# Performance work log

Hardware: AMD Instinct MI355X
Metric: run time of the kernel (lower is better)

Reference implementation:

```python
import jax, jax.numpy as jnp
import numpy as np
import math

N = 50000       # nodes
E = 800000      # edges
C_IN = 64
C_OUT = 32
N_SH = 9        # (l_max+1)^2 with l_max=2
H = 32          # radial_hidden_dim


def spherical_harmonics(vectors):
    # vectors: [..., 3] -> [..., 9]; faithful to source incl. (x+iy).real == x
    norm = jnp.clip(jnp.linalg.norm(vectors, axis=-1, keepdims=True), 1e-8)
    d = vectors / norm
    x, y, z = d[..., 0], d[..., 1], d[..., 2]
    c00 = 0.5 / math.sqrt(math.pi)
    c1 = 0.5 * math.sqrt(3.0 / (2.0 * math.pi))
    c1z = 0.5 * math.sqrt(3.0 / math.pi)
    c2 = 0.25 * math.sqrt(15.0 / (2.0 * math.pi))
    c2z = 0.5 * math.sqrt(15.0 / (2.0 * math.pi))
    c20 = 0.25 * math.sqrt(5.0 / math.pi)
    feats = [
        c00 * jnp.ones_like(x),
        -c1 * x,                      # -0.5*sqrt(3/2pi)*(x+iy).real
        c1z * z,
        c1 * x,                       # 0.5*sqrt(3/2pi)*(x-iy).real
        c2 * (x * x - y * y),         # 0.25*sqrt(15/2pi)*((x+iy)^2).real
        -c2z * z * x,
        c20 * (2.0 * z * z - x * x - y * y),
        c2z * z * x,
        c2 * (x * x - y * y),
    ]
    return jnp.stack(feats, axis=-1)


def setup_inputs() -> dict:
    key = jax.random.key(0)
    ks = jax.random.split(key, 9)
    features = jax.random.normal(ks[0], (N, C_IN), dtype=jnp.float32)
    positions = jax.random.normal(ks[1], (N, 3), dtype=jnp.float32)
    edge_index = jax.random.randint(ks[2], (2, E), 0, N, dtype=jnp.int64)
    fan1 = N_SH + C_IN  # 73 (intended fan-in of first radial layer)
    W1 = jax.random.normal(ks[3], (fan1, H), dtype=jnp.float32) / math.sqrt(fan1)
    b1 = jnp.zeros((H,), dtype=jnp.float32)
    W2 = jax.random.normal(ks[4], (H, H), dtype=jnp.float32) / math.sqrt(H)
    b2 = jnp.zeros((H,), dtype=jnp.float32)
    W3 = jax.random.normal(ks[5], (H, N_SH * C_OUT), dtype=jnp.float32) / math.sqrt(H)
    b3 = jnp.zeros((N_SH * C_OUT,), dtype=jnp.float32)
    return {"features": features, "positions": positions, "W1": W1, "b1": b1,
            "W2": W2, "b2": b2, "W3": W3, "b3": b3, "edge_index": edge_index}


def reference(features, positions, W1, b1, W2, b2, W3, b3, edge_index):
    row, col = edge_index[0], edge_index[1]
    rel_pos = positions[row] - positions[col]                 # [E,3]
    dist = jnp.clip(jnp.linalg.norm(rel_pos, axis=-1, keepdims=True), 1e-8)
    directions = rel_pos / dist
    y_ij = spherical_harmonics(directions)                    # [E,9]
    combined = jnp.concatenate([y_ij, features[col]], axis=-1)  # [E,9+C_IN]
    h = jax.nn.silu(combined @ W1 + b1)
    h = jax.nn.silu(h @ W2 + b2)
    messages = h @ W3 + b3                                    # [E,9*C_OUT]
    msg = messages.reshape(-1, N_SH, C_OUT).sum(axis=1)       # [E,C_OUT]
    out = jax.ops.segment_sum(msg, row, num_segments=features.shape[0])
    return out
```

## Files before the change

kernel.cpp:

```cpp
#include <hip/hip_runtime.h>
#include <hip/hip_fp16.h>

#define NNODES 50000
#define NEDGES 800000
#define CIN 64
#define COUT 32
#define NSH 9
#define HDIM 32

#define NT_BLOCKS 6250
#define HIST_BLOCKS 782
#define SCAN_BLOCKS 125
#define SCAN_CHUNK 400

__device__ __forceinline__ void prep_body(
    int t, const float* __restrict__ W3, const float* __restrict__ b3,
    const float* __restrict__ W1, const float* __restrict__ b1,
    float* __restrict__ W3s, float* __restrict__ b3s, float* __restrict__ prm)
{
    if (t < HDIM * COUT) {
        int k = t >> 5, c = t & 31;
        float s = 0.f;
        #pragma unroll
        for (int q = 0; q < NSH; ++q) s += W3[k * (NSH * COUT) + q * COUT + c];
        W3s[t] = s;
    }
    if (t < COUT) {
        float s = 0.f;
        #pragma unroll
        for (int q = 0; q < NSH; ++q) s += b3[q * COUT + t];
        b3s[t] = s;
    }
    if (t < HDIM) {
        const float c00 = 0.28209479177387814f;
        const float c1  = 0.3454941494713355f;
        const float c1z = 0.4886025119029199f;
        const float c2  = 0.38627420202318958f;
        const float c2z = 0.7725484040463791f;
        const float c20 = 0.31539156525252005f;
        prm[t]       = b1[t] + c00 * W1[0 * HDIM + t];
        prm[32 + t]  = c1  * (W1[3 * HDIM + t] - W1[1 * HDIM + t]);
        prm[64 + t]  = c1z *  W1[2 * HDIM + t];
        prm[96 + t]  = c2z * (W1[7 * HDIM + t] - W1[5 * HDIM + t]);
        prm[128 + t] = c2  * (W1[4 * HDIM + t] + W1[8 * HDIM + t]);
        prm[160 + t] = c20 *  W1[6 * HDIM + t];
    }
}

__global__ void prep_w3(const float* __restrict__ W3, const float* __restrict__ b3,
                        const float* __restrict__ W1, const float* __restrict__ b1,
                        float* __restrict__ W3s, float* __restrict__ b3s,
                        float* __restrict__ prm) {
    prep_body(threadIdx.x, W3, b3, W1, b1, W3s, b3s, prm);
}

__global__ __launch_bounds__(256) void nt_hist(
    const float* __restrict__ feat, const float* __restrict__ W1,
    const int* __restrict__ ei, float* __restrict__ g1,
    int* __restrict__ cnt, int do_nt)
{
    int b = blockIdx.x;
    if (do_nt && b < NT_BLOCKS) {
        int tid = b * 256 + threadIdx.x;
        int n = tid >> 5, c = tid & 31;
        if (n < NNODES) {
            float acc = 0.f;
            const float* fr = feat + (size_t)n * CIN;
            const float* wp = W1 + NSH * HDIM + c;
            #pragma unroll 8
            for (int k = 0; k < CIN; ++k)
                acc = fmaf(fr[k], wp[k * HDIM], acc);
            g1[(size_t)n * HDIM + c] = acc;
        }
    } else {
        int hb = do_nt ? (b - NT_BLOCKS) : b;
        int e4 = (hb * 256 + threadIdx.x) * 4;
        if (e4 < NEDGES) {
            int4 r = *reinterpret_cast<const int4*>(ei + e4);
            atomicAdd(&cnt[r.x], 1);
            atomicAdd(&cnt[r.y], 1);
            atomicAdd(&cnt[r.z], 1);
            atomicAdd(&cnt[r.w], 1);
        }
    }
}

__global__ __launch_bounds__(256) void scan_bsum(const int* __restrict__ cnt,
                                                 int* __restrict__ bsum) {
    int b = blockIdx.x, t = threadIdx.x;
    int base = b * SCAN_CHUNK;
    int s = 0;
    for (int i = t; i < SCAN_CHUNK; i += 256) s += cnt[base + i];
    #pragma unroll
    for (int d = 32; d > 0; d >>= 1) s += __shfl_down(s, d);
    __shared__ int l4[4];
    if ((t & 63) == 0) l4[t >> 6] = s;
    __syncthreads();
    if (t == 0) bsum[b] = l4[0] + l4[1] + l4[2] + l4[3];
}

__global__ __launch_bounds__(1024) void scan_top_prep(
    const int* __restrict__ bsum, int* __restrict__ ebsum, int* __restrict__ off,
    const float* __restrict__ W3, const float* __restrict__ b3,
    const float* __restrict__ W1, const float* __restrict__ b1,
    float* __restrict__ W3s, float* __restrict__ b3s, float* __restrict__ prm)
{
    if (blockIdx.x == 1) {
        prep_body(threadIdx.x, W3, b3, W1, b1, W3s, b3s, prm);
        return;
    }
    __shared__ int lds[128];
    int t = threadIdx.x;
    if (t < 128) lds[t] = (t < SCAN_BLOCKS) ? bsum[t] : 0;
    __syncthreads();
    for (int d = 1; d < 128; d <<= 1) {
        int u = (t >= d && t < 128) ? lds[t - d] : 0;
        __syncthreads();
        if (t < 128) lds[t] += u;
        __syncthreads();
    }
    if (t < SCAN_BLOCKS) ebsum[t] = (t == 0) ? 0 : lds[t - 1];
    if (t == 0) off[NNODES] = NEDGES;
}

__global__ __launch_bounds__(256) void scan_offsets(const int* __restrict__ cnt,
                                                    const int* __restrict__ ebsum,
                                                    int* __restrict__ off,
                                                    int* __restrict__ cursor) {
    int b = blockIdx.x, t = threadIdx.x;
    int base = b * SCAN_CHUNK;
    __shared__ int lds[256];
    int2 c2 = make_int2(0, 0);
    if (t < SCAN_CHUNK / 2) c2 = reinterpret_cast<const int2*>(cnt + base)[t];
    int ps = c2.x + c2.y;
    lds[t] = ps;
    __syncthreads();
    for (int d = 1; d < 256; d <<= 1) {
        int u = (t >= d) ? lds[t - d] : 0;
        __syncthreads();
        lds[t] += u;
        __syncthreads();
    }
    int excl = lds[t] - ps;
    if (t < SCAN_CHUNK / 2) {
        int o = ebsum[b] + excl;
        int2 w = make_int2(o, o + c2.x);
        reinterpret_cast<int2*>(off + base)[t] = w;
        reinterpret_cast<int2*>(cursor + base)[t] = w;
    }
}

__global__ __launch_bounds__(256) void edge_compute_g1(
    const float* __restrict__ g1, const float* __restrict__ pos,
    const float* __restrict__ prm,
    const float* __restrict__ W2, const float* __restrict__ b2,
    const float* __restrict__ W3s, const float* __restrict__ b3s,
    const int* __restrict__ ei, int* __restrict__ cursor,
    unsigned int* __restrict__ msg)
{
    int e = blockIdx.x * blockDim.x + threadIdx.x;
    if (e >= NEDGES) return;
    int row = ei[e];
    int col = ei[NEDGES + e];

    int slot = atomicAdd(&cursor[row], 1);
    unsigned int* mp = msg + (size_t)slot * 16;

    float px = pos[3 * row + 0] - pos[3 * col + 0];
    float py = pos[3 * row + 1] - pos[3 * col + 1];
    float pz = pos[3 * row + 2] - pos[3 * col + 2];
    float dist = fmaxf(sqrtf(px * px + py * py + pz * pz), 1e-8f);
    float inv = 1.0f / dist;
    float dx = px * inv, dy = py * inv, dz = pz * inv;
    float n2 = fmaxf(sqrtf(dx * dx + dy * dy + dz * dz), 1e-8f);
    float i2 = 1.0f / n2;
    float x = dx * i2, y = dy * i2, z = dz * i2;

    float zx = z * x;
    float xxyy = x * x - y * y;
    float w6 = 2.f * z * z - x * x - y * y;

    const float* b1e = prm;
    const float* A = prm + 32;
    const float* B = prm + 64;
    const float* C = prm + 96;
    const float* D = prm + 128;
    const float* E = prm + 160;

    float h1[HDIM];
    const float4* g4 = reinterpret_cast<const float4*>(g1 + (size_t)col * HDIM);
    #pragma unroll
    for (int q = 0; q < 8; ++q) {
        float4 g = g4[q];
        h1[4 * q + 0] = g.x; h1[4 * q + 1] = g.y;
        h1[4 * q + 2] = g.z; h1[4 * q + 3] = g.w;
    }
    #pragma unroll
    for (int c = 0; c < HDIM; ++c) {
        float v = h1[c] + b1e[c];
        v = fmaf(x, A[c], v);
        v = fmaf(z, B[c], v);
        v = fmaf(zx, C[c], v);
        v = fmaf(xxyy, D[c], v);
        v = fmaf(w6, E[c], v);
        h1[c] = v / (1.f + __expf(-v));
    }

    float h2[HDIM];
    #pragma unroll
    for (int c = 0; c < HDIM; ++c) h2[c] = b2[c];
    for (int k = 0; k < HDIM; ++k) {
        float v = h1[k];
        #pragma unroll
        for (int c = 0; c < HDIM; ++c) h2[c] = fmaf(v, W2[k * HDIM + c], h2[c]);
    }
    #pragma unroll
    for (int c = 0; c < HDIM; ++c) {
        float v = h2[c];
        h2[c] = v / (1.f + __expf(-v));
    }

    float m[COUT];
    #pragma unroll
    for (int c = 0; c < COUT; ++c) m[c] = b3s[c];
    for (int k = 0; k < HDIM; ++k) {
        float v = h2[k];
        #pragma unroll
        for (int c = 0; c < COUT; ++c) m[c] = fmaf(v, W3s[k * COUT + c], m[c]);
    }

    uint4 pk[4];
    unsigned int* pu = reinterpret_cast<unsigned int*>(pk);
    #pragma unroll
    for (int q = 0; q < 16; ++q) {
        __half2 hh = __floats2half2_rn(m[2 * q], m[2 * q + 1]);
        pu[q] = *reinterpret_cast<unsigned int*>(&hh);
    }
    uint4* mp4 = reinterpret_cast<uint4*>(mp);
    #pragma unroll
    for (int q = 0; q < 4; ++q) mp4[q] = pk[q];
}

__global__ __launch_bounds__(256) void gather_kernel(
    const unsigned int* __restrict__ msg, const int* __restrict__ off,
    float* __restrict__ out)
{
    int node = blockIdx.x * 4 + (threadIdx.x >> 6);
    if (node >= NNODES) return;
    int lane = threadIdx.x & 63;
    int g = lane >> 4, p = lane & 15;
    int s0 = off[node], s1 = off[node + 1];
    float ax = 0.f, ay = 0.f;
    for (int s = s0 + g; s < s1; s += 4) {
        unsigned int u = msg[(size_t)s * 16 + p];
        __half2 h = *reinterpret_cast<__half2*>(&u);
        ax += __low2float(h);
        ay += __high2float(h);
    }
    ax += __shfl_xor(ax, 16); ay += __shfl_xor(ay, 16);
    ax += __shfl_xor(ax, 32); ay += __shfl_xor(ay, 32);
    if (lane < 16)
        reinterpret_cast<float2*>(out + (size_t)node * COUT)[p] = make_float2(ax, ay);
}

__global__ __launch_bounds__(256) void edge_atomic_kernel(
    const float* __restrict__ feat, const float* __restrict__ pos,
    const float* __restrict__ W1, const float* __restrict__ b1,
    const float* __restrict__ W2, const float* __restrict__ b2,
    const float* __restrict__ W3s, const float* __restrict__ b3s,
    const int* __restrict__ ei, float* __restrict__ out)
{
    int e = blockIdx.x * blockDim.x + threadIdx.x;
    if (e >= NEDGES) return;
    int row = ei[e];
    int col = ei[NEDGES + e];

    float px = pos[3 * row + 0] - pos[3 * col + 0];
    float py = pos[3 * row + 1] - pos[3 * col + 1];
    float pz = pos[3 * row + 2] - pos[3 * col + 2];
    float dist = fmaxf(sqrtf(px * px + py * py + pz * pz), 1e-8f);
    float inv = 1.0f / dist;
    float dx = px * inv, dy = py * inv, dz = pz * inv;
    float n2 = fmaxf(sqrtf(dx * dx + dy * dy + dz * dz), 1e-8f);
    float i2 = 1.0f / n2;
    float x = dx * i2, y = dy * i2, z = dz * i2;

    const float c00 = 0.28209479177387814f;
    const float c1  = 0.3454941494713355f;
    const float c1z = 0.4886025119029199f;
    const float c2  = 0.38627420202318958f;
    const float c2z = 0.7725484040463791f;
    const float c20 = 0.31539156525252005f;

    float sh[NSH];
    float xxyy = x * x - y * y;
    float zx = z * x;
    sh[0] = c00;
    sh[1] = -c1 * x;
    sh[2] = c1z * z;
    sh[3] = c1 * x;
    sh[4] = c2 * xxyy;
    sh[5] = -c2z * zx;
    sh[6] = c20 * (2.f * z * z - x * x - y * y);
    sh[7] = c2z * zx;
    sh[8] = c2 * xxyy;

    float h1[HDIM];
    #pragma unroll
    for (int c = 0; c < HDIM; ++c) h1[c] = b1[c];
    #pragma unroll
    for (int k = 0; k < NSH; ++k) {
        float v = sh[k];
        #pragma unroll
        for (int c = 0; c < HDIM; ++c) h1[c] = fmaf(v, W1[k * HDIM + c], h1[c]);
    }
    const float4* f4 = reinterpret_cast<const float4*>(feat + (size_t)col * CIN);
    for (int kk = 0; kk < CIN / 4; ++kk) {
        float4 f = f4[kk];
        const float* Wp = W1 + (NSH + kk * 4) * HDIM;
        #pragma unroll
        for (int c = 0; c < HDIM; ++c) h1[c] = fmaf(f.x, Wp[c], h1[c]);
        #pragma unroll
        for (int c = 0; c < HDIM; ++c) h1[c] = fmaf(f.y, Wp[HDIM + c], h1[c]);
        #pragma unroll
        for (int c = 0; c < HDIM; ++c) h1[c] = fmaf(f.z, Wp[2 * HDIM + c], h1[c]);
        #pragma unroll
        for (int c = 0; c < HDIM; ++c) h1[c] = fmaf(f.w, Wp[3 * HDIM + c], h1[c]);
    }
    #pragma unroll
    for (int c = 0; c < HDIM; ++c) {
        float v = h1[c];
        h1[c] = v / (1.f + __expf(-v));
    }

    float h2[HDIM];
    #pragma unroll
    for (int c = 0; c < HDIM; ++c) h2[c] = b2[c];
    for (int k = 0; k < HDIM; ++k) {
        float v = h1[k];
        #pragma unroll
        for (int c = 0; c < HDIM; ++c) h2[c] = fmaf(v, W2[k * HDIM + c], h2[c]);
    }
    #pragma unroll
    for (int c = 0; c < HDIM; ++c) {
        float v = h2[c];
        h2[c] = v / (1.f + __expf(-v));
    }

    float m[COUT];
    #pragma unroll
    for (int c = 0; c < COUT; ++c) m[c] = b3s[c];
    for (int k = 0; k < HDIM; ++k) {
        float v = h2[k];
        #pragma unroll
        for (int c = 0; c < COUT; ++c) m[c] = fmaf(v, W3s[k * COUT + c], m[c]);
    }

    float* op = out + (size_t)row * COUT;
    #pragma unroll
    for (int c = 0; c < COUT; ++c) atomicAdd(op + c, m[c]);
}

extern "C" void kernel_launch(void* const* d_in, const int* in_sizes, int n_in,
                              void* d_out, int out_size, void* d_ws, size_t ws_size,
                              hipStream_t stream) {
    const float* feat = (const float*)d_in[0];
    const float* pos  = (const float*)d_in[1];
    const float* W1   = (const float*)d_in[2];
    const float* b1   = (const float*)d_in[3];
    const float* W2   = (const float*)d_in[4];
    const float* b2   = (const float*)d_in[5];
    const float* W3   = (const float*)d_in[6];
    const float* b3   = (const float*)d_in[7];
    const int*   ei   = (const int*)d_in[8];
    float* outf = (float*)d_out;

    int* cnt    = (int*)d_ws;
    int* off    = cnt + NNODES;
    int* cursor = off + NNODES + 2;
    int* bsum   = cursor + NNODES;
    int* ebsum  = bsum + 128;
    const size_t head_ints = ((size_t)NNODES + (NNODES + 2) + NNODES + 128 + 128 + 3) & ~(size_t)3;
    float* fbase = (float*)(((int*)d_ws) + head_ints);
    float* W3s = fbase;
    float* b3s = W3s + HDIM * COUT;
    float* prm = b3s + COUT;
    const size_t head_floats = HDIM * COUT + COUT + 192;
    float* g1 = fbase + head_floats;
    unsigned int* msg = (unsigned int*)(g1 + (size_t)NNODES * HDIM);
    size_t need = (head_ints + head_floats + (size_t)NNODES * HDIM) * 4
                + (size_t)NEDGES * 16 * 4;

    if (ws_size >= need) {
        (void)hipMemsetAsync(cnt, 0, (size_t)NNODES * sizeof(int), stream);
        nt_hist<<<NT_BLOCKS + HIST_BLOCKS, 256, 0, stream>>>(feat, W1, ei, g1, cnt, 1);
        scan_bsum<<<SCAN_BLOCKS, 256, 0, stream>>>(cnt, bsum);
        scan_top_prep<<<2, 1024, 0, stream>>>(bsum, ebsum, off, W3, b3, W1, b1, W3s, b3s, prm);
        scan_offsets<<<SCAN_BLOCKS, 256, 0, stream>>>(cnt, ebsum, off, cursor);
        edge_compute_g1<<<(NEDGES + 255) / 256, 256, 0, stream>>>(
            g1, pos, prm, W2, b2, W3s, b3s, ei, cursor, msg);
        gather_kernel<<<(NNODES + 3) / 4, 256, 0, stream>>>(msg, off, outf);
    } else {
        (void)hipMemsetAsync(d_out, 0, (size_t)out_size * sizeof(float), stream);
        prep_w3<<<1, 1024, 0, stream>>>(W3, b3, W1, b1, W3s, b3s, prm);
        edge_atomic_kernel<<<(NEDGES + 255) / 256, 256, 0, stream>>>(
            feat, pos, W1, b1, W2, b2, W3s, b3s, ei, outf);
    }
}
```

Measured before the change: 160.8 us.

## Sort edges by destination via permutation and store node projections in fp16

Adds a separate pass that scatters edge indices into a destination-sorted permutation, so the edge kernel processes edges in sorted order and writes messages contiguously instead of to atomically-claimed scattered slots. The per-node first-layer projection g1 is now stored as half precision, halving the bytes of the random gather by column. The cost is an extra kernel launch, extra permutation reads, scattered reads of edge indices and positions in permuted order, and reduced precision of the hidden pre-activations.

```diff
diff --git a/kernel.cpp b/kernel.cpp
--- a/kernel.cpp
+++ b/kernel.cpp
@@ -56,7 +56,7 @@
 
 __global__ __launch_bounds__(256) void nt_hist(
     const float* __restrict__ feat, const float* __restrict__ W1,
-    const int* __restrict__ ei, float* __restrict__ g1,
+    const int* __restrict__ ei, __half* __restrict__ g1h,
     int* __restrict__ cnt, int do_nt)
 {
     int b = blockIdx.x;
@@ -70,7 +70,7 @@
             #pragma unroll 8
             for (int k = 0; k < CIN; ++k)
                 acc = fmaf(fr[k], wp[k * HDIM], acc);
-            g1[(size_t)n * HDIM + c] = acc;
+            g1h[(size_t)n * HDIM + c] = __float2half(acc);
         }
     } else {
         int hb = do_nt ? (b - NT_BLOCKS) : b;
@@ -150,21 +150,30 @@
     }
 }
 
-__global__ __launch_bounds__(256) void edge_compute_g1(
-    const float* __restrict__ g1, const float* __restrict__ pos,
+__global__ __launch_bounds__(256) void perm_scatter(const int* __restrict__ ei,
+                                                    int* __restrict__ cursor,
+                                                    int* __restrict__ perm) {
+    int e = blockIdx.x * 256 + threadIdx.x;
+    if (e < NEDGES) {
+        int row = ei[e];
+        int slot = atomicAdd(&cursor[row], 1);
+        perm[slot] = e;
+    }
+}
+
+__global__ __launch_bounds__(256) void edge_compute_sorted(
+    const __half* __restrict__ g1h, const float* __restrict__ pos,
     const float* __restrict__ prm,
     const float* __restrict__ W2, const float* __restrict__ b2,
     const float* __restrict__ W3s, const float* __restrict__ b3s,
-    const int* __restrict__ ei, int* __restrict__ cursor,
+    const int* __restrict__ ei, const int* __restrict__ perm,
     unsigned int* __restrict__ msg)
 {
-    int e = blockIdx.x * blockDim.x + threadIdx.x;
-    if (e >= NEDGES) return;
+    int i = blockIdx.x * blockDim.x + threadIdx.x;
+    if (i >= NEDGES) return;
+    int e = perm[i];
     int row = ei[e];
     int col = ei[NEDGES + e];
-
-    int slot = atomicAdd(&cursor[row], 1);
-    unsigned int* mp = msg + (size_t)slot * 16;
 
     float px = pos[3 * row + 0] - pos[3 * col + 0];
     float py = pos[3 * row + 1] - pos[3 * col + 1];
@@ -188,12 +197,17 @@
     const float* E = prm + 160;
 
     float h1[HDIM];
-    const float4* g4 = reinterpret_cast<const float4*>(g1 + (size_t)col * HDIM);
-    #pragma unroll
-    for (int q = 0; q < 8; ++q) {
-        float4 g = g4[q];
-        h1[4 * q + 0] = g.x; h1[4 * q + 1] = g.y;
-        h1[4 * q + 2] = g.z; h1[4 * q + 3] = g.w;
+    const uint4* g4 = reinterpret_cast<const uint4*>(g1h + (size_t)col * HDIM);
+    #pragma unroll
+    for (int q = 0; q < 4; ++q) {
+        uint4 u = g4[q];
+        const unsigned int uw[4] = {u.x, u.y, u.z, u.w};
+        #pragma unroll
+        for (int j = 0; j < 4; ++j) {
+            __half2 h = *reinterpret_cast<const __half2*>(&uw[j]);
+            h1[8 * q + 2 * j]     = __low2float(h);
+            h1[8 * q + 2 * j + 1] = __high2float(h);
+        }
     }
     #pragma unroll
     for (int c = 0; c < HDIM; ++c) {
@@ -236,7 +250,7 @@
         __half2 hh = __floats2half2_rn(m[2 * q], m[2 * q + 1]);
         pu[q] = *reinterpret_cast<unsigned int*>(&hh);
     }
-    uint4* mp4 = reinterpret_cast<uint4*>(mp);
+    uint4* mp4 = reinterpret_cast<uint4*>(msg + (size_t)i * 16);
     #pragma unroll
     for (int q = 0; q < 4; ++q) mp4[q] = pk[q];
 }
@@ -380,25 +394,29 @@
     int* cursor = off + NNODES + 2;
     int* bsum   = cursor + NNODES;
     int* ebsum  = bsum + 128;
-    const size_t head_ints = ((size_t)NNODES + (NNODES + 2) + NNODES + 128 + 128 + 3) & ~(size_t)3;
+    int* perm   = ebsum + 128;
+    const size_t head_ints = ((size_t)NNODES + (NNODES + 2) + NNODES + 128 + 128
+                              + NEDGES + 3) & ~(size_t)3;
     float* fbase = (float*)(((int*)d_ws) + head_ints);
     float* W3s = fbase;
     float* b3s = W3s + HDIM * COUT;
     float* prm = b3s + COUT;
     const size_t head_floats = HDIM * COUT + COUT + 192;
-    float* g1 = fbase + head_floats;
-    unsigned int* msg = (unsigned int*)(g1 + (size_t)NNODES * HDIM);
-    size_t need = (head_ints + head_floats + (size_t)NNODES * HDIM) * 4
-                + (size_t)NEDGES * 16 * 4;
+    __half* g1h = (__half*)(fbase + head_floats);
+    unsigned int* msg = (unsigned int*)(g1h + (size_t)NNODES * HDIM);
+    size_t need = (head_ints + head_floats) * 4
+                + (size_t)NNODES * HDIM * 2
+                + (size_t)NEDGES * 64;
 
     if (ws_size >= need) {
         (void)hipMemsetAsync(cnt, 0, (size_t)NNODES * sizeof(int), stream);
-        nt_hist<<<NT_BLOCKS + HIST_BLOCKS, 256, 0, stream>>>(feat, W1, ei, g1, cnt, 1);
+        nt_hist<<<NT_BLOCKS + HIST_BLOCKS, 256, 0, stream>>>(feat, W1, ei, g1h, cnt, 1);
         scan_bsum<<<SCAN_BLOCKS, 256, 0, stream>>>(cnt, bsum);
         scan_top_prep<<<2, 1024, 0, stream>>>(bsum, ebsum, off, W3, b3, W1, b1, W3s, b3s, prm);
         scan_offsets<<<SCAN_BLOCKS, 256, 0, stream>>>(cnt, ebsum, off, cursor);
-        edge_compute_g1<<<(NEDGES + 255) / 256, 256, 0, stream>>>(
-            g1, pos, prm, W2, b2, W3s, b3s, ei, cursor, msg);
+        perm_scatter<<<(NEDGES + 255) / 256, 256, 0, stream>>>(ei, cursor, perm);
+        edge_compute_sorted<<<(NEDGES + 255) / 256, 256, 0, stream>>>(
+            g1h, pos, prm, W2, b2, W3s, b3s, ei, perm, msg);
         gather_kernel<<<(NNODES + 3) / 4, 256, 0, stream>>>(msg, off, outf);
     } else {
         (void)hipMemsetAsync(d_out, 0, (size_t)out_size * sizeof(float), stream);
```

Result: slower. 216.6 us (+34.8%).
